# Kernel optimization log

Hardware: AMD Instinct MI355X
Metric: run time of the kernel (lower is better)

Reference implementation:

```python
import jax, jax.numpy as jnp
import numpy as np

N_EMBED = 1024
N_HEADS = 16
HEAD_SIZE = N_EMBED // N_HEADS
B, T = 4, 2048
LN_EPS = 1e-5


def _layer_norm(x, gamma, beta):
    mu = jnp.mean(x, axis=-1, keepdims=True)
    var = jnp.var(x, axis=-1, keepdims=True)
    return (x - mu) * jax.lax.rsqrt(var + LN_EPS) * gamma + beta


def setup_inputs() -> dict:
    key = jax.random.key(0)
    ks = jax.random.split(key, 12)
    s = 1.0 / np.sqrt(N_EMBED)
    sh = 1.0 / np.sqrt(4 * N_EMBED)
    return {
        "x": jax.random.normal(ks[0], (B, T, N_EMBED), jnp.float32),
        "Wk": jax.random.uniform(ks[1], (N_EMBED, N_EMBED), jnp.float32, -s, s),
        "Wq": jax.random.uniform(ks[2], (N_EMBED, N_EMBED), jnp.float32, -s, s),
        "Wv": jax.random.uniform(ks[3], (N_EMBED, N_EMBED), jnp.float32, -s, s),
        "Wproj": jax.random.uniform(ks[4], (N_EMBED, N_EMBED), jnp.float32, -s, s),
        "bproj": jax.random.uniform(ks[5], (N_EMBED,), jnp.float32, -s, s),
        "W1": jax.random.uniform(ks[6], (N_EMBED, 4 * N_EMBED), jnp.float32, -s, s),
        "b1": jax.random.uniform(ks[7], (4 * N_EMBED,), jnp.float32, -s, s),
        "W2": jax.random.uniform(ks[8], (4 * N_EMBED, N_EMBED), jnp.float32, -sh, sh),
        "b2": jax.random.uniform(ks[9], (N_EMBED,), jnp.float32, -sh, sh),
        "g1": jnp.ones((N_EMBED,), jnp.float32),
        "beta1": jnp.zeros((N_EMBED,), jnp.float32),
        "g2": jnp.ones((N_EMBED,), jnp.float32),
        "beta2": jnp.zeros((N_EMBED,), jnp.float32),
    }


def reference(x, Wk, Wq, Wv, Wproj, bproj, W1, b1, W2, b2, g1, beta1, g2, beta2):
    Bt, Tt, C = x.shape
    h = _layer_norm(x, g1, beta1)
    # project and split heads: (B, H, T, D)
    def heads(W):
        return (h @ W).reshape(Bt, Tt, N_HEADS, HEAD_SIZE).transpose(0, 2, 1, 3)
    q, k, v = heads(Wq), heads(Wk), heads(Wv)
    wei = jnp.einsum("bhtd,bhsd->bhts", q, k) / np.sqrt(HEAD_SIZE)
    causal = jnp.tril(jnp.ones((Tt, Tt), bool))
    wei = jnp.where(causal, wei, -jnp.inf)
    wei = jax.nn.softmax(wei, axis=-1)
    out = jnp.einsum("bhts,bhsd->bhtd", wei, v)
    out = out.transpose(0, 2, 1, 3).reshape(Bt, Tt, C)
    x = x + out @ Wproj + bproj
    h2 = _layer_norm(x, g2, beta2)
    ff = jax.nn.relu(h2 @ W1 + b1) @ W2 + b2
    return x + ff
```

## Files before the change

kernel.cpp:

```cpp
#include <hip/hip_runtime.h>
#include <stdint.h>

typedef __bf16 bf16x8 __attribute__((ext_vector_type(8)));
typedef float f32x4 __attribute__((ext_vector_type(4)));
typedef unsigned short u16x8 __attribute__((ext_vector_type(8)));
typedef unsigned short u16x4 __attribute__((ext_vector_type(4)));
typedef unsigned int u32x2 __attribute__((ext_vector_type(2)));
typedef float fvec4 __attribute__((ext_vector_type(4)));

__device__ __forceinline__ unsigned short f2b(float f) {
  unsigned u = __builtin_bit_cast(unsigned, f);
  return (unsigned short)((u + 0x7fffu + ((u >> 16) & 1u)) >> 16);
}

__device__ __forceinline__ bf16x8 ldfrag(const unsigned short* p) {
  return __builtin_bit_cast(bf16x8, *(const u16x8*)p);
}

__device__ __forceinline__ float fexp2(float x) {
  float r;
  asm("v_exp_f32 %0, %1" : "=v"(r) : "v"(x));
  return r;
}

__device__ __forceinline__ unsigned cvtpk(float a, float b) {
  unsigned r;
  asm("v_cvt_pk_bf16_f32 %0, %1, %2" : "=v"(r) : "v"(a), "v"(b));
  return r;
}

__device__ __forceinline__ void gload_lds16(const void* g, void* l) {
  auto gp = reinterpret_cast<const __attribute__((address_space(1))) void*>(
      reinterpret_cast<uintptr_t>(g));
  auto lp = reinterpret_cast<__attribute__((address_space(3))) void*>(
      reinterpret_cast<uintptr_t>(l));
  __builtin_amdgcn_global_load_lds(gp, lp, 16, 0, 0);
}

__global__ void transpose_cast(const float* __restrict__ W, unsigned short* __restrict__ Wt,
                               int K, int N) {
  __shared__ float tile[32][33];
  const int n0 = blockIdx.x * 32, k0 = blockIdx.y * 32;
  const int tx = threadIdx.x, ty = threadIdx.y;
#pragma unroll
  for (int j = 0; j < 4; ++j)
    tile[ty + j * 8][tx] = W[(size_t)(k0 + ty + j * 8) * N + n0 + tx];
  __syncthreads();
#pragma unroll
  for (int j = 0; j < 4; ++j)
    Wt[(size_t)(n0 + ty + j * 8) * K + k0 + tx] = f2b(tile[tx][ty + j * 8]);
}

__global__ void ln_kernel(const float* __restrict__ X, const float* __restrict__ g,
                          const float* __restrict__ be, unsigned short* __restrict__ H) {
  const int row = (blockIdx.x * blockDim.x + threadIdx.x) >> 6;
  const int l = threadIdx.x & 63;
  const float* xr = X + (size_t)row * 1024;
  fvec4 v[4];
  float s = 0.f, sq = 0.f;
#pragma unroll
  for (int i = 0; i < 4; ++i) {
    v[i] = *(const fvec4*)(xr + i * 256 + l * 4);
#pragma unroll
    for (int j = 0; j < 4; ++j) { s += v[i][j]; sq += v[i][j] * v[i][j]; }
  }
#pragma unroll
  for (int off = 32; off >= 1; off >>= 1) {
    s += __shfl_xor(s, off);
    sq += __shfl_xor(sq, off);
  }
  const float mean = s * (1.f / 1024.f);
  const float var = sq * (1.f / 1024.f) - mean * mean;
  const float rstd = rsqrtf(var + 1e-5f);
#pragma unroll
  for (int i = 0; i < 4; ++i) {
    const int col = i * 256 + l * 4;
    fvec4 gg = *(const fvec4*)(g + col);
    fvec4 bb = *(const fvec4*)(be + col);
    u16x4 o;
#pragma unroll
    for (int j = 0; j < 4; ++j) o[j] = f2b((v[i][j] - mean) * rstd * gg[j] + bb[j]);
    *(u16x4*)(H + (size_t)row * 1024 + col) = o;
  }
}

template <int EPI>
__global__ __launch_bounds__(512, 1) void gemmS(
    const unsigned short* __restrict__ A, const unsigned short* __restrict__ Bt,
    const float* __restrict__ bias, const float* __restrict__ resid,
    float* __restrict__ Cf, unsigned short* __restrict__ Cb,
    unsigned short* __restrict__ pK, unsigned short* __restrict__ pVT,
    int N, int K, int ntiles) {
  constexpr int ASZ = 16384;
  constexpr int BSZ = 32768;
  constexpr int BUFSZ = ASZ + BSZ;
  __shared__ __align__(16) char lds[3 * BUFSZ];

  const int tid = threadIdx.x;
  const int w = tid >> 6, l = tid & 63;
  const int wr = w >> 2, wc = w & 3;
  const int kg = l >> 4, fr = l & 15;
  const int xtiles = N / 256;
  const int nblk = (int)gridDim.x;

  int Aoff[2][4], Boff[2][4];
#pragma unroll
  for (int kk = 0; kk < 2; ++kk) {
#pragma unroll
    for (int m = 0; m < 4; ++m) {
      const int r = wr * 64 + m * 16 + fr;
      Aoff[kk][m] = r * 128 + (((kk * 4 + kg) ^ (r & 7)) << 4);
    }
#pragma unroll
    for (int n = 0; n < 4; ++n) {
      const int rn = wc * 64 + n * 16 + fr;
      Boff[kk][n] = ASZ + rn * 128 + (((kk * 4 + kg) ^ (rn & 7)) << 4);
    }
  }

  for (int tl = (int)blockIdx.x; tl < ntiles; tl += nblk) {
    if (tl != (int)blockIdx.x) __builtin_amdgcn_s_barrier();
    const int q8 = ntiles >> 3;
    const int swz = (tl & 7) * q8 + (tl >> 3);
    const size_t am0 = (size_t)(swz / xtiles) * 128;
    const size_t bn0 = (size_t)(swz % xtiles) * 256;

    const char* src[6];
#pragma unroll
    for (int u = 0; u < 2; ++u) {
      const int flat = u * 512 + tid;
      const int row = flat >> 3, c = flat & 7;
      src[u] = (const char*)(A + (am0 + row) * K) + ((c ^ (row & 7)) << 4);
    }
#pragma unroll
    for (int u = 0; u < 4; ++u) {
      const int flat = u * 512 + tid;
      const int row = flat >> 3, c = flat & 7;
      src[2 + u] = (const char*)(Bt + (bn0 + row) * K) + ((c ^ (row & 7)) << 4);
    }

    f32x4 acc[4][4];
#pragma unroll
    for (int m = 0; m < 4; ++m)
#pragma unroll
      for (int n = 0; n < 4; ++n) acc[m][n] = (f32x4){0.f, 0.f, 0.f, 0.f};

    auto stage = [&](int sb) {
      char* Ld = lds + sb * BUFSZ;
#pragma unroll
      for (int u = 0; u < 2; ++u) {
        gload_lds16(src[u], Ld + u * 8192 + tid * 16);
        src[u] += 128;
      }
#pragma unroll
      for (int u = 0; u < 4; ++u) {
        gload_lds16(src[2 + u], Ld + ASZ + u * 8192 + tid * 16);
        src[2 + u] += 128;
      }
    };

    const int NT = K >> 6;
    stage(0);
    stage(1);
    asm volatile("s_waitcnt vmcnt(6)" ::: "memory");
    __builtin_amdgcn_s_barrier();

    int cb0 = 0, sb = 2;
    for (int kt = 0; kt < NT; ++kt) {
      if (kt + 2 < NT) stage(sb);
#pragma unroll
      for (int kk = 0; kk < 2; ++kk) {
        bf16x8 af[4], bf[4];
#pragma unroll
        for (int m = 0; m < 4; ++m)
          af[m] = ldfrag((const unsigned short*)(lds + cb0 + Aoff[kk][m]));
#pragma unroll
        for (int n = 0; n < 4; ++n)
          bf[n] = ldfrag((const unsigned short*)(lds + cb0 + Boff[kk][n]));
        __builtin_amdgcn_s_setprio(1);
#pragma unroll
        for (int m = 0; m < 4; ++m)
#pragma unroll
          for (int n = 0; n < 4; ++n)
            acc[m][n] = __builtin_amdgcn_mfma_f32_16x16x32_bf16(af[m], bf[n], acc[m][n], 0, 0, 0);
        __builtin_amdgcn_s_setprio(0);
      }
      if (kt + 2 < NT) {
        asm volatile("s_waitcnt vmcnt(6)" ::: "memory");
        __builtin_amdgcn_s_barrier();
      } else if (kt + 1 < NT) {
        asm volatile("s_waitcnt vmcnt(0)" ::: "memory");
        __builtin_amdgcn_s_barrier();
      }
      cb0 += BUFSZ;
      if (cb0 == 3 * BUFSZ) cb0 = 0;
      sb += 1;
      if (sb == 3) sb = 0;
    }

#pragma unroll
    for (int m = 0; m < 4; ++m) {
      const size_t row0 = am0 + wr * 64 + m * 16 + kg * 4;
#pragma unroll
      for (int n = 0; n < 4; ++n) {
        const size_t col = bn0 + wc * 64 + n * 16 + fr;
        if (EPI == 3) {
          if (bn0 < 1024) {
#pragma unroll
            for (int r = 0; r < 4; ++r) Cb[(row0 + r) * 1024 + col] = f2b(acc[m][n][r]);
          } else if (bn0 < 2048) {
#pragma unroll
            for (int r = 0; r < 4; ++r) pK[(row0 + r) * 1024 + col - 1024] = f2b(acc[m][n][r]);
          } else {
            const int c2 = (int)col - 2048;
            const int hh = c2 >> 6, dd = c2 & 63;
            const int bb = (int)(row0 >> 11), tt = (int)(row0 & 2047);
            u16x4 pv;
#pragma unroll
            for (int r = 0; r < 4; ++r) pv[r] = f2b(acc[m][n][r]);
            *(u16x4*)(pVT + (((size_t)bb * 16 + hh) * 64 + dd) * 2048 + tt) = pv;
          }
        } else {
          const float bv = (EPI >= 1) ? bias[col] : 0.f;
#pragma unroll
          for (int r = 0; r < 4; ++r) {
            const size_t idx = (row0 + r) * N + col;
            float v = acc[m][n][r] + bv;
            if (EPI == 1) v = fmaxf(v, 0.f);
            if (EPI == 2) {
              Cf[idx] = v + resid[idx];
            } else {
              Cb[idx] = f2b(v);
            }
          }
        }
      }
    }
  }
}

#define PSTR 72
#define SC2 0.18033688f
__global__ __launch_bounds__(256, 2) void attn_kernel(const unsigned short* __restrict__ Qb,
                                                      const unsigned short* __restrict__ Kb,
                                                      const unsigned short* __restrict__ VT,
                                                      unsigned short* __restrict__ ATT) {
  __shared__ __align__(16) char ldsK[3 * 8192];
  __shared__ __align__(16) unsigned short Pl[4][64 * PSTR];
  const int tid = threadIdx.x;
  const int w = tid >> 6, l = tid & 63;
  const int kg = l >> 4, fr = l & 15;
  const int bh = blockIdx.x;
  const int b = bh >> 4, h = bh & 15;
  const int yy = (int)blockIdx.y;
  const int qt = (yy < 4) ? 7 - yy : yy - 4;
  const int q0 = qt * 256 + w * 64;
  const size_t rbase = (size_t)b * 2048;
  const unsigned short* vtb = VT + (size_t)bh * 64 * 2048;
  const f32x4 fz = {0.f, 0.f, 0.f, 0.f};

  const int rowoff = tid >> 3;
  const int cbsw = ((tid & 7) * 16) ^ ((rowoff & 7) << 4);
  const char* ksrc = (const char*)(Kb + rbase * 1024 + h * 64) + (size_t)rowoff * 2048 + cbsw;

  int koff[4][2];
#pragma unroll
  for (int sg = 0; sg < 4; ++sg)
#pragma unroll
    for (int c = 0; c < 2; ++c)
      koff[sg][c] = (sg * 16 + fr) * 128 + ((c * 64 + kg * 16) ^ ((fr & 7) << 4));

  bf16x8 bq[4][2];
#pragma unroll
  for (int qg = 0; qg < 4; ++qg) {
    const unsigned short* qrow = Qb + (rbase + q0 + qg * 16 + fr) * 1024 + h * 64;
#pragma unroll
    for (int c = 0; c < 2; ++c) bq[qg][c] = ldfrag(qrow + c * 32 + kg * 8);
  }

  f32x4 o[4][4];
#pragma unroll
  for (int qg = 0; qg < 4; ++qg)
#pragma unroll
    for (int nd = 0; nd < 4; ++nd) o[qg][nd] = (f32x4){0.f, 0.f, 0.f, 0.f};
  float m_run2[4] = {-1e30f, -1e30f, -1e30f, -1e30f};
  float l_run[4] = {0.f, 0.f, 0.f, 0.f};

  auto stage = [&](int t, int sbuf) {
    gload_lds16(ksrc + (size_t)(t * 64) * 2048, ldsK + sbuf * 8192 + tid * 16);
    gload_lds16(ksrc + (size_t)(t * 64 + 32) * 2048, ldsK + sbuf * 8192 + 4096 + tid * 16);
  };

  auto softmax_qg = [&](int qg, int s0, f32x4 (&stq)[4]) -> float {
    const int qa = q0 + qg * 16 + fr;
    float vals[16];
    if (s0 + 63 <= q0 + qg * 16) {
#pragma unroll
      for (int sg = 0; sg < 4; ++sg)
#pragma unroll
        for (int r = 0; r < 4; ++r) vals[sg * 4 + r] = stq[sg][r];
    } else {
#pragma unroll
      for (int sg = 0; sg < 4; ++sg)
#pragma unroll
        for (int r = 0; r < 4; ++r) {
          const int sa = s0 + sg * 16 + kg * 4 + r;
          vals[sg * 4 + r] = (sa > qa) ? -1e30f : stq[sg][r];
        }
    }
    float m5[5];
#pragma unroll
    for (int i = 0; i < 5; ++i)
      m5[i] = fmaxf(fmaxf(vals[3 * i], vals[3 * i + 1]), vals[3 * i + 2]);
    const float vmax =
        fmaxf(fmaxf(fmaxf(m5[0], m5[1]), m5[2]), fmaxf(fmaxf(m5[3], m5[4]), vals[15]));
    const float tm2 = vmax * SC2;
    if (__any(tm2 > m_run2[qg] + 8.f)) {
      float tmax2 = tm2;
      tmax2 = fmaxf(tmax2, __shfl_xor(tmax2, 16));
      tmax2 = fmaxf(tmax2, __shfl_xor(tmax2, 32));
      const float m_new2 = fmaxf(m_run2[qg], tmax2);
      const float alpha = fexp2(m_run2[qg] - m_new2);
      m_run2[qg] = m_new2;
      l_run[qg] *= alpha;
      float al[4];
#pragma unroll
      for (int r = 0; r < 4; ++r) al[r] = __shfl(alpha, kg * 4 + r);
#pragma unroll
      for (int nd = 0; nd < 4; ++nd)
#pragma unroll
        for (int r = 0; r < 4; ++r) o[qg][nd][r] *= al[r];
    }
    const float nm2 = -m_run2[qg];
    float psum = 0.f;
    unsigned pk[8];
#pragma unroll
    for (int i = 0; i < 8; ++i) {
      const float p0 = fexp2(__builtin_fmaf(vals[2 * i], SC2, nm2));
      const float p1 = fexp2(__builtin_fmaf(vals[2 * i + 1], SC2, nm2));
      psum += p0 + p1;
      pk[i] = cvtpk(p0, p1);
    }
#pragma unroll
    for (int sg = 0; sg < 4; ++sg) {
      u32x2 w2 = {pk[2 * sg], pk[2 * sg + 1]};
      *(u32x2*)(&Pl[w][(qg * 16 + fr) * PSTR + sg * 16 + kg * 4]) = w2;
    }
    return psum;
  };

  auto compute = [&](int s0, int cbb) {
    if (s0 > q0 + 63) return;
    bf16x8 vb[4][2];
#pragma unroll
    for (int nd = 0; nd < 4; ++nd)
#pragma unroll
      for (int ks = 0; ks < 2; ++ks)
        vb[nd][ks] = ldfrag(vtb + (size_t)(nd * 16 + fr) * 2048 + s0 + ks * 32 + kg * 8);

    float psv[4];
#pragma unroll
    for (int qp = 0; qp < 2; ++qp) {
      f32x4 st[4][2];
#pragma unroll
      for (int sg = 0; sg < 4; ++sg) {
        const bf16x8 ka0 = ldfrag((const unsigned short*)(ldsK + cbb + koff[sg][0]));
        const bf16x8 ka1 = ldfrag((const unsigned short*)(ldsK + cbb + koff[sg][1]));
#pragma unroll
        for (int qh = 0; qh < 2; ++qh)
          st[sg][qh] = __builtin_amdgcn_mfma_f32_16x16x32_bf16(
              ka1, bq[qp * 2 + qh][1],
              __builtin_amdgcn_mfma_f32_16x16x32_bf16(ka0, bq[qp * 2 + qh][0], fz, 0, 0, 0),
              0, 0, 0);
      }
#pragma unroll
      for (int qh = 0; qh < 2; ++qh) {
        f32x4 stq[4];
#pragma unroll
        for (int sg = 0; sg < 4; ++sg) stq[sg] = st[sg][qh];
        psv[qp * 2 + qh] = softmax_qg(qp * 2 + qh, s0, stq);
      }
    }

    {
      float a[4], c[4];
#pragma unroll
      for (int qg = 0; qg < 4; ++qg) a[qg] = __shfl_xor(psv[qg], 16);
#pragma unroll
      for (int qg = 0; qg < 4; ++qg) psv[qg] += a[qg];
#pragma unroll
      for (int qg = 0; qg < 4; ++qg) c[qg] = __shfl_xor(psv[qg], 32);
#pragma unroll
      for (int qg = 0; qg < 4; ++qg) l_run[qg] += psv[qg] + c[qg];
    }

#pragma unroll
    for (int qg = 0; qg < 4; ++qg)
#pragma unroll
      for (int ks = 0; ks < 2; ++ks) {
        const bf16x8 pa = ldfrag(&Pl[w][(qg * 16 + fr) * PSTR + ks * 32 + kg * 8]);
#pragma unroll
        for (int nd = 0; nd < 4; ++nd)
          o[qg][nd] = __builtin_amdgcn_mfma_f32_16x16x32_bf16(pa, vb[nd][ks], o[qg][nd], 0, 0, 0);
      }
  };

  const int NT = 4 * qt + 4;
  stage(0, 0);
  stage(1, 1);
  asm volatile("s_waitcnt vmcnt(2)" ::: "memory");
  __builtin_amdgcn_s_barrier();
  int cb = 0, sb = 2;
  for (int t = 0; t < NT; ++t) {
    if (t + 2 < NT) stage(t + 2, sb);
    compute(t * 64, cb * 8192);
    if (t + 2 < NT) {
      asm volatile("s_waitcnt vmcnt(2)" ::: "memory");
      __builtin_amdgcn_s_barrier();
    } else if (t + 1 < NT) {
      asm volatile("s_waitcnt vmcnt(0)" ::: "memory");
      __builtin_amdgcn_s_barrier();
    }
    cb += 1; if (cb == 3) cb = 0;
    sb += 1; if (sb == 3) sb = 0;
  }

#pragma unroll
  for (int qg = 0; qg < 4; ++qg) {
    const float li = __builtin_amdgcn_rcpf(l_run[qg]);
    float linv[4];
#pragma unroll
    for (int r = 0; r < 4; ++r) linv[r] = __shfl(li, kg * 4 + r);
#pragma unroll
    for (int nd = 0; nd < 4; ++nd)
#pragma unroll
      for (int r = 0; r < 4; ++r) {
        const size_t row = rbase + q0 + qg * 16 + kg * 4 + r;
        ATT[row * 1024 + h * 64 + nd * 16 + fr] = f2b(o[qg][nd][r] * linv[r]);
      }
  }
}

extern "C" void kernel_launch(void* const* d_in, const int* in_sizes, int n_in, void* d_out,
                              int out_size, void* d_ws, size_t ws_size, hipStream_t stream) {
  const float* x = (const float*)d_in[0];
  const float* Wk = (const float*)d_in[1];
  const float* Wq = (const float*)d_in[2];
  const float* Wv = (const float*)d_in[3];
  const float* Wproj = (const float*)d_in[4];
  const float* bproj = (const float*)d_in[5];
  const float* W1 = (const float*)d_in[6];
  const float* b1 = (const float*)d_in[7];
  const float* W2 = (const float*)d_in[8];
  const float* b2 = (const float*)d_in[9];
  const float* g1 = (const float*)d_in[10];
  const float* beta1 = (const float*)d_in[11];
  const float* g2 = (const float*)d_in[12];
  const float* beta2 = (const float*)d_in[13];
  float* out = (float*)d_out;
  unsigned short* wsu = (unsigned short*)d_ws;

  const size_t o_qkvW = 0;
  const size_t o_projW = o_qkvW + 3072 * 1024;
  const size_t o_W1 = o_projW + 1024 * 1024;
  const size_t o_W2 = o_W1 + 4096 * 1024;
  const size_t o_H = o_W2 + 1024 * 4096;
  const size_t o_Q = o_H + (size_t)8192 * 1024;
  const size_t o_K = o_Q + (size_t)8192 * 1024;
  const size_t o_VT = o_K + (size_t)8192 * 1024;
  const size_t o_ATT = o_VT + (size_t)8192 * 1024;
  const size_t o_FF1 = o_Q;

  dim3 tpb(32, 8);
  transpose_cast<<<dim3(32, 32), tpb, 0, stream>>>(Wq, wsu + o_qkvW, 1024, 1024);
  transpose_cast<<<dim3(32, 32), tpb, 0, stream>>>(Wk, wsu + o_qkvW + 1024 * 1024, 1024, 1024);
  transpose_cast<<<dim3(32, 32), tpb, 0, stream>>>(Wv, wsu + o_qkvW + 2 * 1024 * 1024, 1024, 1024);
  transpose_cast<<<dim3(32, 32), tpb, 0, stream>>>(Wproj, wsu + o_projW, 1024, 1024);
  transpose_cast<<<dim3(128, 32), tpb, 0, stream>>>(W1, wsu + o_W1, 1024, 4096);
  transpose_cast<<<dim3(32, 128), tpb, 0, stream>>>(W2, wsu + o_W2, 4096, 1024);

  ln_kernel<<<2048, 256, 0, stream>>>(x, g1, beta1, wsu + o_H);

  gemmS<3><<<256, 512, 0, stream>>>(wsu + o_H, wsu + o_qkvW, nullptr, nullptr, nullptr,
                                    wsu + o_Q, wsu + o_K, wsu + o_VT, 3072, 1024, 768);

  attn_kernel<<<dim3(64, 8), 256, 0, stream>>>(wsu + o_Q, wsu + o_K, wsu + o_VT, wsu + o_ATT);

  gemmS<2><<<256, 512, 0, stream>>>(wsu + o_ATT, wsu + o_projW, bproj, x, out, nullptr,
                                    nullptr, nullptr, 1024, 1024, 256);

  ln_kernel<<<2048, 256, 0, stream>>>(out, g2, beta2, wsu + o_H);

  gemmS<1><<<256, 512, 0, stream>>>(wsu + o_H, wsu + o_W1, b1, nullptr, nullptr,
                                    wsu + o_FF1, nullptr, nullptr, 4096, 1024, 1024);

  gemmS<2><<<256, 512, 0, stream>>>(wsu + o_FF1, wsu + o_W2, b2, out, out, nullptr,
                                    nullptr, nullptr, 1024, 4096, 256);
}
```

Measured before the change: 340.6 us.

## Add BK=32 four-stage GEMM for QKV and shrink attention P buffer

Adds a new GEMM kernel with a 32-wide K step, a 4-deep LDS ring and a templated M tile, and uses it (BM=128) for the QKV projection instead of the 3-stage BK=64 kernel. The EPI==3 epilogue is removed from the old kernel. Attention now finishes the softmax and PV MFMAs per pair of query groups, which halves the per-wave P buffer in LDS and allows three blocks per CU. The new GEMM doubles the number of barriers per K and uses smaller tiles. Higher attention occupancy adds register pressure.

```diff
diff --git a/kernel.cpp b/kernel.cpp
--- a/kernel.cpp
+++ b/kernel.cpp
@@ -81,6 +81,154 @@
 #pragma unroll
     for (int j = 0; j < 4; ++j) o[j] = f2b((v[i][j] - mean) * rstd * gg[j] + bb[j]);
     *(u16x4*)(H + (size_t)row * 1024 + col) = o;
+  }
+}
+
+template <int BM, int EPI>
+__global__ __launch_bounds__(512, 1) void gemm32(
+    const unsigned short* __restrict__ A, const unsigned short* __restrict__ Bt,
+    const float* __restrict__ bias, const float* __restrict__ resid,
+    float* __restrict__ Cf, unsigned short* __restrict__ Cb,
+    unsigned short* __restrict__ pK, unsigned short* __restrict__ pVT,
+    int N, int K, int ntiles) {
+  constexpr int ASZ = BM * 64;
+  constexpr int BSZ = 16384;
+  constexpr int BUFSZ = ASZ + BSZ;
+  constexpr int UA = ASZ / 8192;
+  constexpr int UNITS = UA + 2;
+  constexpr int MF = BM / 32;
+  __shared__ __align__(16) char lds[4 * BUFSZ];
+
+  const int tid = threadIdx.x;
+  const int w = tid >> 6, l = tid & 63;
+  const int wr = w >> 2, wc = w & 3;
+  const int kg = l >> 4, fr = l & 15;
+  const int xtiles = N / 256;
+  const int nblk = (int)gridDim.x;
+
+  int Aoff[MF], Boff[4];
+#pragma unroll
+  for (int m = 0; m < MF; ++m) {
+    const int r = wr * (BM / 2) + m * 16 + fr;
+    Aoff[m] = r * 64 + ((kg ^ ((r >> 1) & 3)) << 4);
+  }
+#pragma unroll
+  for (int n = 0; n < 4; ++n) {
+    const int rn = wc * 64 + n * 16 + fr;
+    Boff[n] = ASZ + rn * 64 + ((kg ^ ((rn >> 1) & 3)) << 4);
+  }
+
+  for (int tl = (int)blockIdx.x; tl < ntiles; tl += nblk) {
+    if (tl != (int)blockIdx.x) __builtin_amdgcn_s_barrier();
+    const int q8 = ntiles >> 3;
+    const int swz = (tl & 7) * q8 + (tl >> 3);
+    const size_t am0 = (size_t)(swz / xtiles) * BM;
+    const size_t bn0 = (size_t)(swz % xtiles) * 256;
+
+    const char* src[UNITS];
+#pragma unroll
+    for (int u = 0; u < UA; ++u) {
+      const int flat = u * 512 + tid;
+      const int row = flat >> 2;
+      const int scb = ((flat & 3) << 4) ^ (((row >> 1) & 3) << 4);
+      src[u] = (const char*)(A + (am0 + row) * K) + scb;
+    }
+#pragma unroll
+    for (int u = 0; u < 2; ++u) {
+      const int flat = u * 512 + tid;
+      const int row = flat >> 2;
+      const int scb = ((flat & 3) << 4) ^ (((row >> 1) & 3) << 4);
+      src[UA + u] = (const char*)(Bt + (bn0 + row) * K) + scb;
+    }
+
+    f32x4 acc[MF][4];
+#pragma unroll
+    for (int m = 0; m < MF; ++m)
+#pragma unroll
+      for (int n = 0; n < 4; ++n) acc[m][n] = (f32x4){0.f, 0.f, 0.f, 0.f};
+
+    auto stage = [&](int sb) {
+#pragma unroll
+      for (int u = 0; u < UNITS; ++u) {
+        gload_lds16(src[u], lds + sb * BUFSZ + u * 8192 + tid * 16);
+        src[u] += 64;
+      }
+    };
+
+    const int NT = K >> 5;
+    stage(0);
+    stage(1);
+    asm volatile("s_waitcnt vmcnt(%0)" ::"i"(UNITS) : "memory");
+    __builtin_amdgcn_s_barrier();
+
+    int cb0 = 0, sb = 2;
+    for (int kt = 0; kt < NT; ++kt) {
+      if (kt + 2 < NT) stage(sb);
+      bf16x8 af[MF], bf[4];
+#pragma unroll
+      for (int m = 0; m < MF; ++m)
+        af[m] = ldfrag((const unsigned short*)(lds + cb0 + Aoff[m]));
+#pragma unroll
+      for (int n = 0; n < 4; ++n)
+        bf[n] = ldfrag((const unsigned short*)(lds + cb0 + Boff[n]));
+      __builtin_amdgcn_s_setprio(1);
+#pragma unroll
+      for (int m = 0; m < MF; ++m)
+#pragma unroll
+        for (int n = 0; n < 4; ++n)
+          acc[m][n] = __builtin_amdgcn_mfma_f32_16x16x32_bf16(af[m], bf[n], acc[m][n], 0, 0, 0);
+      __builtin_amdgcn_s_setprio(0);
+      if (kt + 2 < NT) {
+        asm volatile("s_waitcnt vmcnt(%0)" ::"i"(UNITS) : "memory");
+        __builtin_amdgcn_s_barrier();
+      } else if (kt + 1 < NT) {
+        asm volatile("s_waitcnt vmcnt(0)" ::: "memory");
+        __builtin_amdgcn_s_barrier();
+      }
+      cb0 += BUFSZ;
+      if (cb0 == 4 * BUFSZ) cb0 = 0;
+      sb += 1;
+      if (sb == 4) sb = 0;
+    }
+
+#pragma unroll
+    for (int m = 0; m < MF; ++m) {
+      const size_t row0 = am0 + wr * (BM / 2) + m * 16 + kg * 4;
+#pragma unroll
+      for (int n = 0; n < 4; ++n) {
+        const size_t col = bn0 + wc * 64 + n * 16 + fr;
+        if (EPI == 3) {
+          if (bn0 < 1024) {
+#pragma unroll
+            for (int r = 0; r < 4; ++r) Cb[(row0 + r) * 1024 + col] = f2b(acc[m][n][r]);
+          } else if (bn0 < 2048) {
+#pragma unroll
+            for (int r = 0; r < 4; ++r) pK[(row0 + r) * 1024 + col - 1024] = f2b(acc[m][n][r]);
+          } else {
+            const int c2 = (int)col - 2048;
+            const int hh = c2 >> 6, dd = c2 & 63;
+            const int bb = (int)(row0 >> 11), tt = (int)(row0 & 2047);
+            u16x4 pv;
+#pragma unroll
+            for (int r = 0; r < 4; ++r) pv[r] = f2b(acc[m][n][r]);
+            *(u16x4*)(pVT + (((size_t)bb * 16 + hh) * 64 + dd) * 2048 + tt) = pv;
+          }
+        } else {
+          const float bv = (EPI >= 1) ? bias[col] : 0.f;
+#pragma unroll
+          for (int r = 0; r < 4; ++r) {
+            const size_t idx = (row0 + r) * N + col;
+            float v = acc[m][n][r] + bv;
+            if (EPI == 1) v = fmaxf(v, 0.f);
+            if (EPI == 2) {
+              Cf[idx] = v + resid[idx];
+            } else {
+              Cb[idx] = f2b(v);
+            }
+          }
+        }
+      }
+    }
   }
 }
 
@@ -204,34 +352,16 @@
 #pragma unroll
       for (int n = 0; n < 4; ++n) {
         const size_t col = bn0 + wc * 64 + n * 16 + fr;
-        if (EPI == 3) {
-          if (bn0 < 1024) {
-#pragma unroll
-            for (int r = 0; r < 4; ++r) Cb[(row0 + r) * 1024 + col] = f2b(acc[m][n][r]);
-          } else if (bn0 < 2048) {
-#pragma unroll
-            for (int r = 0; r < 4; ++r) pK[(row0 + r) * 1024 + col - 1024] = f2b(acc[m][n][r]);
+        const float bv = (EPI >= 1) ? bias[col] : 0.f;
+#pragma unroll
+        for (int r = 0; r < 4; ++r) {
+          const size_t idx = (row0 + r) * N + col;
+          float v = acc[m][n][r] + bv;
+          if (EPI == 1) v = fmaxf(v, 0.f);
+          if (EPI == 2) {
+            Cf[idx] = v + resid[idx];
           } else {
-            const int c2 = (int)col - 2048;
-            const int hh = c2 >> 6, dd = c2 & 63;
-            const int bb = (int)(row0 >> 11), tt = (int)(row0 & 2047);
-            u16x4 pv;
-#pragma unroll
-            for (int r = 0; r < 4; ++r) pv[r] = f2b(acc[m][n][r]);
-            *(u16x4*)(pVT + (((size_t)bb * 16 + hh) * 64 + dd) * 2048 + tt) = pv;
-          }
-        } else {
-          const float bv = (EPI >= 1) ? bias[col] : 0.f;
-#pragma unroll
-          for (int r = 0; r < 4; ++r) {
-            const size_t idx = (row0 + r) * N + col;
-            float v = acc[m][n][r] + bv;
-            if (EPI == 1) v = fmaxf(v, 0.f);
-            if (EPI == 2) {
-              Cf[idx] = v + resid[idx];
-            } else {
-              Cb[idx] = f2b(v);
-            }
+            Cb[idx] = f2b(v);
           }
         }
       }
@@ -241,12 +371,12 @@
 
 #define PSTR 72
 #define SC2 0.18033688f
-__global__ __launch_bounds__(256, 2) void attn_kernel(const unsigned short* __restrict__ Qb,
+__global__ __launch_bounds__(256, 3) void attn_kernel(const unsigned short* __restrict__ Qb,
                                                       const unsigned short* __restrict__ Kb,
                                                       const unsigned short* __restrict__ VT,
                                                       unsigned short* __restrict__ ATT) {
   __shared__ __align__(16) char ldsK[3 * 8192];
-  __shared__ __align__(16) unsigned short Pl[4][64 * PSTR];
+  __shared__ __align__(16) unsigned short Pl[4][32 * PSTR];
   const int tid = threadIdx.x;
   const int w = tid >> 6, l = tid & 63;
   const int kg = l >> 4, fr = l & 15;
@@ -291,7 +421,7 @@
     gload_lds16(ksrc + (size_t)(t * 64 + 32) * 2048, ldsK + sbuf * 8192 + 4096 + tid * 16);
   };
 
-  auto softmax_qg = [&](int qg, int s0, f32x4 (&stq)[4]) -> float {
+  auto softmax_qg = [&](int qg, int qh, int s0, f32x4 (&stq)[4]) -> float {
     const int qa = q0 + qg * 16 + fr;
     float vals[16];
     if (s0 + 63 <= q0 + qg * 16) {
@@ -344,7 +474,7 @@
 #pragma unroll
     for (int sg = 0; sg < 4; ++sg) {
       u32x2 w2 = {pk[2 * sg], pk[2 * sg + 1]};
-      *(u32x2*)(&Pl[w][(qg * 16 + fr) * PSTR + sg * 16 + kg * 4]) = w2;
+      *(u32x2*)(&Pl[w][(qh * 16 + fr) * PSTR + sg * 16 + kg * 4]) = w2;
     }
     return psum;
   };
@@ -358,7 +488,6 @@
       for (int ks = 0; ks < 2; ++ks)
         vb[nd][ks] = ldfrag(vtb + (size_t)(nd * 16 + fr) * 2048 + s0 + ks * 32 + kg * 8);
 
-    float psv[4];
 #pragma unroll
     for (int qp = 0; qp < 2; ++qp) {
       f32x4 st[4][2];
@@ -373,36 +502,35 @@
               __builtin_amdgcn_mfma_f32_16x16x32_bf16(ka0, bq[qp * 2 + qh][0], fz, 0, 0, 0),
               0, 0, 0);
       }
+      float psv[2];
 #pragma unroll
       for (int qh = 0; qh < 2; ++qh) {
         f32x4 stq[4];
 #pragma unroll
         for (int sg = 0; sg < 4; ++sg) stq[sg] = st[sg][qh];
-        psv[qp * 2 + qh] = softmax_qg(qp * 2 + qh, s0, stq);
-      }
-    }
-
-    {
-      float a[4], c[4];
-#pragma unroll
-      for (int qg = 0; qg < 4; ++qg) a[qg] = __shfl_xor(psv[qg], 16);
-#pragma unroll
-      for (int qg = 0; qg < 4; ++qg) psv[qg] += a[qg];
-#pragma unroll
-      for (int qg = 0; qg < 4; ++qg) c[qg] = __shfl_xor(psv[qg], 32);
-#pragma unroll
-      for (int qg = 0; qg < 4; ++qg) l_run[qg] += psv[qg] + c[qg];
-    }
-
-#pragma unroll
-    for (int qg = 0; qg < 4; ++qg)
-#pragma unroll
-      for (int ks = 0; ks < 2; ++ks) {
-        const bf16x8 pa = ldfrag(&Pl[w][(qg * 16 + fr) * PSTR + ks * 32 + kg * 8]);
-#pragma unroll
-        for (int nd = 0; nd < 4; ++nd)
-          o[qg][nd] = __builtin_amdgcn_mfma_f32_16x16x32_bf16(pa, vb[nd][ks], o[qg][nd], 0, 0, 0);
-      }
+        psv[qh] = softmax_qg(qp * 2 + qh, qh, s0, stq);
+      }
+      {
+        const float a0 = __shfl_xor(psv[0], 16);
+        const float a1 = __shfl_xor(psv[1], 16);
+        psv[0] += a0;
+        psv[1] += a1;
+        const float b0 = __shfl_xor(psv[0], 32);
+        const float b1 = __shfl_xor(psv[1], 32);
+        l_run[qp * 2] += psv[0] + b0;
+        l_run[qp * 2 + 1] += psv[1] + b1;
+      }
+#pragma unroll
+      for (int qh = 0; qh < 2; ++qh)
+#pragma unroll
+        for (int ks = 0; ks < 2; ++ks) {
+          const bf16x8 pa = ldfrag(&Pl[w][(qh * 16 + fr) * PSTR + ks * 32 + kg * 8]);
+#pragma unroll
+          for (int nd = 0; nd < 4; ++nd)
+            o[qp * 2 + qh][nd] =
+                __builtin_amdgcn_mfma_f32_16x16x32_bf16(pa, vb[nd][ks], o[qp * 2 + qh][nd], 0, 0, 0);
+        }
+    }
   };
 
   const int NT = 4 * qt + 4;
@@ -481,8 +609,8 @@
 
   ln_kernel<<<2048, 256, 0, stream>>>(x, g1, beta1, wsu + o_H);
 
-  gemmS<3><<<256, 512, 0, stream>>>(wsu + o_H, wsu + o_qkvW, nullptr, nullptr, nullptr,
-                                    wsu + o_Q, wsu + o_K, wsu + o_VT, 3072, 1024, 768);
+  gemm32<128, 3><<<256, 512, 0, stream>>>(wsu + o_H, wsu + o_qkvW, nullptr, nullptr, nullptr,
+                                          wsu + o_Q, wsu + o_K, wsu + o_VT, 3072, 1024, 768);
 
   attn_kernel<<<dim3(64, 8), 256, 0, stream>>>(wsu + o_Q, wsu + o_K, wsu + o_VT, wsu + o_ATT);
 
```

Measured after the change: 520.0 us. 52.7% more time.
